# Performance work log

Hardware: AMD Instinct MI355X
Metric: run time of the kernel (lower is better)

Reference implementation:

```python
import jax, jax.numpy as jnp
import numpy as np
from jax import lax

T, B, DIN, H, OUT, L = 256, 128, 20, 1024, 1095, 3


def setup_inputs() -> dict:
    key = jax.random.key(0)
    ks = jax.random.split(key, 8)
    x = jax.random.normal(ks[0], (T, B, DIN), dtype=jnp.float32)
    c = jnp.zeros((L, B, H), dtype=jnp.float32)  # accepted but unused, as in original
    s_in = 1.0 / np.sqrt(DIN)
    s_h = 1.0 / np.sqrt(H)
    W1 = jax.random.uniform(ks[1], (DIN, H), jnp.float32, -s_in, s_in)
    b1 = jnp.zeros((H,), jnp.float32)
    # SRU per-layer weights: W maps h -> [z | f_pre | r_pre] (3H); biases for f and r gates
    W_sru = jax.random.uniform(ks[2], (L, H, 3 * H), jnp.float32, -s_h, s_h)
    bf_sru = jnp.zeros((L, H), jnp.float32)
    br_sru = jnp.zeros((L, H), jnp.float32)
    W3 = jax.random.uniform(ks[3], (H, OUT), jnp.float32, -s_h, s_h)
    b3 = jnp.zeros((OUT,), jnp.float32)
    return {"x": x, "c": c, "W1": W1, "b1": b1, "W_sru": W_sru,
            "bf_sru": bf_sru, "br_sru": br_sru, "W3": W3, "b3": b3}


def _sru_layer(h, W, bf, br):
    """One SRU layer. h: (T,B,H). Returns (h_out (T,B,H), c_final (B,H))."""
    U = jnp.einsum('tbh,hk->tbk', h, W)                    # (T,B,3H) big GEMM up front
    z, f_pre, r_pre = jnp.split(U, 3, axis=-1)
    f = jax.nn.sigmoid(f_pre + bf)
    r = jax.nn.sigmoid(r_pre + br)

    def step(c_prev, inp):
        f_t, z_t, r_t, x_t = inp
        c_t = f_t * c_prev + (1.0 - f_t) * z_t
        h_t = r_t * c_t + (1.0 - r_t) * x_t               # highway (input_size == hidden_size)
        return c_t, h_t

    c0 = jnp.zeros(h.shape[1:], h.dtype)
    c_final, h_out = lax.scan(step, c0, (f, z, r, h))
    return h_out, c_final


def reference(x, c, W1, b1, W_sru, bf_sru, br_sru, W3, b3):
    t, b, _ = x.shape
    h = (x.reshape(t * b, -1) @ W1 + b1).reshape(t, b, H)  # Dense_layer1
    c_finals = []
    for l in range(L):                                      # 3 SRU layers (fixed count)
        h, c_l = _sru_layer(h, W_sru[l], bf_sru[l], br_sru[l])
        c_finals.append(c_l)
    out = h.reshape(t * b, H) @ W3 + b3                     # Dense_layer3 -> (T*B, OUT)
    return out, jnp.stack(c_finals)                         # ((T*B,OUT), (L,B,H))
```

## Files before the change

kernel.cpp:

```cpp
#include <hip/hip_runtime.h>
#include <hip/hip_bf16.h>


#define T_DIM 256
#define B_DIM 128
#define DIN 20
#define H_DIM 1024
#define OUT_DIM 1095
#define L_DIM 3
#define M_DIM (T_DIM * B_DIM)
#define H3 (3 * H_DIM)
#define OUT_ELEMS ((size_t)M_DIM * OUT_DIM)

typedef __bf16 bf16x8 __attribute__((ext_vector_type(8)));
typedef __bf16 bf16x4 __attribute__((ext_vector_type(4)));
typedef __bf16 bf16x2 __attribute__((ext_vector_type(2)));
typedef float f32x4 __attribute__((ext_vector_type(4)));

__device__ __forceinline__ void async16(const __bf16* g, __bf16* l) {
  __builtin_amdgcn_global_load_lds(
      (const __attribute__((address_space(1))) void*)g,
      (__attribute__((address_space(3))) void*)l, 16, 0, 0);
}

__global__ void transpose_sru(const float* __restrict__ W, __bf16* __restrict__ Wt) {
  __shared__ float tile[32][33];
  int l = blockIdx.z;
  int j0 = blockIdx.x * 32;
  int i0 = blockIdx.y * 32;
  int tx = threadIdx.x, ty = threadIdx.y;
  const float* Wl = W + (size_t)l * H_DIM * H3;
  __bf16* Wtl = Wt + (size_t)l * H_DIM * H3;
#pragma unroll
  for (int r = 0; r < 4; r++)
    tile[ty + r * 8][tx] = Wl[(size_t)(i0 + ty + r * 8) * H3 + j0 + tx];
  __syncthreads();
#pragma unroll
  for (int r = 0; r < 4; r++)
    Wtl[(size_t)(j0 + ty + r * 8) * H_DIM + i0 + tx] = (__bf16)tile[tx][ty + r * 8];
}

__global__ void transpose_w3(const float* __restrict__ W, __bf16* __restrict__ Wt) {
  __shared__ float tile[32][33];
  int j0 = blockIdx.x * 32;
  int i0 = blockIdx.y * 32;
  int tx = threadIdx.x, ty = threadIdx.y;
#pragma unroll
  for (int r = 0; r < 4; r++) {
    int j = j0 + tx;
    if (j < OUT_DIM)
      tile[ty + r * 8][tx] = W[(size_t)(i0 + ty + r * 8) * OUT_DIM + j];
  }
  __syncthreads();
#pragma unroll
  for (int r = 0; r < 4; r++) {
    int j = j0 + ty + r * 8;
    if (j < OUT_DIM)
      Wt[(size_t)j * H_DIM + i0 + tx] = (__bf16)tile[tx][ty + r * 8];
  }
}

__global__ __launch_bounds__(256) void dense1(const float* __restrict__ x,
                                              const float* __restrict__ W1,
                                              const float* __restrict__ b1,
                                              __bf16* __restrict__ h) {
  __shared__ float wsl[DIN * 256];
  __shared__ float xs[128 * DIN];
  int tid = threadIdx.x;
  int m0 = blockIdx.x * 128;
  int n0 = blockIdx.y * 256;
#pragma unroll
  for (int k = 0; k < DIN; k++) wsl[k * 256 + tid] = W1[k * H_DIM + n0 + tid];
  for (int idx = tid; idx < 128 * DIN; idx += 256) xs[idx] = x[(size_t)m0 * DIN + idx];
  __syncthreads();
  float wreg[DIN];
#pragma unroll
  for (int k = 0; k < DIN; k++) wreg[k] = wsl[k * 256 + tid];
  float bias = b1[n0 + tid];
  for (int m = 0; m < 128; m++) {
    float acc = bias;
#pragma unroll
    for (int k = 0; k < DIN; k++) acc += xs[m * DIN + k] * wreg[k];
    h[(size_t)(m0 + m) * H_DIM + n0 + tid] = (__bf16)acc;
  }
}


template <int MH>
__device__ __forceinline__ void mfma16(f32x4 (&acc)[8][4], const bf16x8 (&aF)[4],
                                       const bf16x8 (&bF)[4]) {
  __builtin_amdgcn_s_setprio(1);
#pragma unroll
  for (int i = 0; i < 4; ++i)
#pragma unroll
    for (int fn = 0; fn < 4; ++fn)
      acc[MH * 4 + i][fn] =
          __builtin_amdgcn_mfma_f32_16x16x32_bf16(bF[fn], aF[i], acc[MH * 4 + i][fn], 0, 0, 0);
  __builtin_amdgcn_s_setprio(0);
}

__global__ __launch_bounds__(512, 2) void gemm_gate(const __bf16* __restrict__ A,
                                                    const __bf16* __restrict__ Bt,
                                                    __bf16* __restrict__ U,
                                                    const float* __restrict__ biasf,
                                                    const float* __restrict__ biasr) {
  __shared__ __align__(16) char lds[131072];
  int tid = threadIdx.x;
  int lane = tid & 63;
  int w = tid >> 6;
  int wm = w & 1, wn = w >> 1;

  int gx = gridDim.x;
  int lin = blockIdx.y * gx + blockIdx.x;
  int xcd = lin & 7;
  int kk = lin >> 3;
  int bx, by;
  if ((gx >> 3) == 8) { bx = xcd * 8 + (kk & 7); by = kk >> 3; }
  else                { bx = xcd * 4 + (kk & 3); by = kk >> 2; }
  int m0 = bx * 256, n0 = by * 256;

  int r8row = w * 8 + (lane >> 3);
  int cse = (lane & 7) * 8;
  int l15 = lane & 15;
  int quad = lane >> 4;

  f32x4 acc[8][4];
#pragma unroll
  for (int i = 0; i < 8; ++i)
#pragma unroll
    for (int j = 0; j < 4; ++j) acc[i][j] = (f32x4)0.f;
  bf16x8 aF[4], bF[4];

#define STAGE_TILE(T_) do { int _t = (T_); int _b = (_t & 1) * 65536;            \
    _Pragma("unroll") for (int _u = 0; _u < 4; ++_u)                             \
      async16(A + (size_t)(m0 + _u * 64 + r8row) * 1024 + _t * 64 + cse,         \
              (__bf16*)(lds + _b + _u * 8192 + w * 1024));                       \
    _Pragma("unroll") for (int _u = 0; _u < 4; ++_u)                             \
      async16(Bt + (size_t)(n0 + _u * 64 + r8row) * 1024 + _t * 64 + cse,        \
              (__bf16*)(lds + _b + 32768 + _u * 8192 + w * 1024)); } while (0)

#define LOAD_A(MH_, KS_) do {                                                    \
    _Pragma("unroll") for (int i = 0; i < 4; ++i)                                \
      aF[i] = *(const bf16x8*)(lds + bufc +                                      \
                (wm * 128 + (MH_) * 64 + i * 16 + l15) * 128 +                   \
                quad * 16 + (KS_) * 64); } while (0)

#define LOAD_B(KS_) do {                                                         \
    _Pragma("unroll") for (int i = 0; i < 4; ++i)                                \
      bF[i] = *(const bf16x8*)(lds + bufc + 32768 +                              \
                (wn * 64 + i * 16 + l15) * 128 +                                 \
                quad * 16 + (KS_) * 64); } while (0)

  STAGE_TILE(0);
  __syncthreads();

#pragma unroll 2
  for (int t = 0; t < 16; ++t) {
    int bufc = (t & 1) * 65536;
    if (t < 15) STAGE_TILE(t + 1);
    LOAD_B(0);
    LOAD_A(0, 0); mfma16<0>(acc, aF, bF);
    LOAD_A(1, 0); mfma16<1>(acc, aF, bF);
    LOAD_B(1);
    LOAD_A(0, 1); mfma16<0>(acc, aF, bF);
    LOAD_A(1, 1); mfma16<1>(acc, aF, bF);
    __syncthreads();
  }
#undef STAGE_TILE
#undef LOAD_A
#undef LOAD_B

  int gN[4];
  f32x4 bV[4];
#pragma unroll
  for (int fn = 0; fn < 4; ++fn) {
    int gc = n0 + wn * 64 + fn * 16 + quad * 4;
    int g = gc >> 10;
    gN[fn] = g;
    if (g == 1) bV[fn] = *(const f32x4*)&biasf[gc - 1024];
    else if (g == 2) bV[fn] = *(const f32x4*)&biasr[gc - 2048];
    else bV[fn] = (f32x4)0.f;
  }
#pragma unroll
  for (int fm = 0; fm < 8; ++fm) {
    int m = wm * 128 + fm * 16 + l15;
    char* rowp = lds + m * 512;
    int msw = (m & 7) << 4;
#pragma unroll
    for (int fn = 0; fn < 4; ++fn) {
      int nq = wn * 64 + fn * 16 + quad * 4;
      f32x4 v = acc[fm][fn];
      if (gN[fn] != 0) {
#pragma unroll
        for (int j = 0; j < 4; ++j) v[j] = 1.f / (1.f + __expf(-(v[j] + bV[fn][j])));
      }
      bf16x4 o;
#pragma unroll
      for (int j = 0; j < 4; ++j) o[j] = (__bf16)v[j];
      *(bf16x4*)(rowp + ((nq * 2) ^ msw)) = o;
    }
  }
  __syncthreads();
#pragma unroll
  for (int it = 0; it < 16; ++it) {
    int idx = it * 512 + tid;
    int row = idx >> 5;
    int ce = (idx & 31) * 8;
    bf16x8 val = *(const bf16x8*)(lds + row * 512 + ((ce * 2) ^ ((row & 7) << 4)));
    *(bf16x8*)&U[(size_t)(m0 + row) * H3 + n0 + ce] = val;
  }
}

__global__ __launch_bounds__(256) void gemm_out(const __bf16* __restrict__ A,
                                                const __bf16* __restrict__ Bt,
                                                float* __restrict__ C,
                                                const float* __restrict__ bias0) {
  constexpr int K = 1024;
  __shared__ __align__(16) __bf16 sA[128 * 32];
  __shared__ __align__(16) __bf16 sB[128 * 32];
  int tid = threadIdx.x;
  int lane = tid & 63;
  int wave = tid >> 6;
  int wm = wave & 1, wn = wave >> 1;
  int m0 = blockIdx.x * 128;
  int n0 = blockIdx.y * 128;

  f32x4 acc[4][4];
#pragma unroll
  for (int i = 0; i < 4; i++)
#pragma unroll
    for (int j = 0; j < 4; j++) acc[i][j] = (f32x4)0.f;

  int lrow = lane >> 2;
  int lcol8 = (lane & 3) * 8;
  int q8 = (lane >> 4) * 8;
  int l15 = lane & 15;

  for (int k0 = 0; k0 < K; k0 += 32) {
    __syncthreads();
#pragma unroll
    for (int i = 0; i < 2; i++) {
      int j = wave * 2 + i;
      int arow = m0 + j * 16 + lrow;
      async16(A + (size_t)arow * K + k0 + lcol8, &sA[j * 512]);
      int brow = n0 + j * 16 + lrow;
      brow = brow < OUT_DIM - 1 ? brow : OUT_DIM - 1;
      async16(Bt + (size_t)brow * K + k0 + lcol8, &sB[j * 512]);
    }
    __syncthreads();
    bf16x8 aF[4], bF[4];
#pragma unroll
    for (int i = 0; i < 4; i++) {
      aF[i] = *(const bf16x8*)&sA[(wm * 64 + i * 16 + l15) * 32 + q8];
      bF[i] = *(const bf16x8*)&sB[(wn * 64 + i * 16 + l15) * 32 + q8];
    }
#pragma unroll
    for (int mi = 0; mi < 4; mi++)
#pragma unroll
      for (int ni = 0; ni < 4; ni++)
        acc[mi][ni] = __builtin_amdgcn_mfma_f32_16x16x32_bf16(aF[mi], bF[ni], acc[mi][ni], 0, 0, 0);
  }

  int quad = lane >> 4;
#pragma unroll
  for (int mi = 0; mi < 4; mi++) {
    int rowBase = m0 + wm * 64 + mi * 16 + quad * 4;
#pragma unroll
    for (int ni = 0; ni < 4; ni++) {
      int col = n0 + wn * 64 + ni * 16 + l15;
      if (col < OUT_DIM) {
        float badd = bias0[col];
#pragma unroll
        for (int r = 0; r < 4; r++)
          C[(size_t)(rowBase + r) * OUT_DIM + col] = acc[mi][ni][r] + badd;
      }
    }
  }
}

__global__ __launch_bounds__(256) void sru_scan(const __bf16* __restrict__ U,
                                                __bf16* __restrict__ h,
                                                float* __restrict__ cst,
                                                float* __restrict__ cfin,
                                                int tc, int first, int last) {
  int id = blockIdx.x * 256 + threadIdx.x;
  int n2 = id * 2;
  int b = n2 >> 10;
  int hh = n2 & 1023;
  float c0, c1;
  if (first) { c0 = 0.f; c1 = 0.f; }
  else { c0 = cst[n2]; c1 = cst[n2 + 1]; }
  size_t ub = (size_t)b * H3 + hh;
  size_t xb = (size_t)b * H_DIM + hh;
  const size_t strideU = (size_t)B_DIM * H3;
  const size_t strideH = (size_t)B_DIM * H_DIM;
  for (int t = 0; t < tc; t++) {
    bf16x2 z2 = *(const bf16x2*)&U[ub];
    bf16x2 f2 = *(const bf16x2*)&U[ub + 1024];
    bf16x2 r2 = *(const bf16x2*)&U[ub + 2048];
    bf16x2 x2 = *(const bf16x2*)&h[xb];
    float f0 = (float)f2[0], f1 = (float)f2[1];
    float r0 = (float)r2[0], r1 = (float)r2[1];
    c0 = f0 * c0 + (1.f - f0) * (float)z2[0];
    c1 = f1 * c1 + (1.f - f1) * (float)z2[1];
    float h0 = r0 * c0 + (1.f - r0) * (float)x2[0];
    float h1 = r1 * c1 + (1.f - r1) * (float)x2[1];
    bf16x2 o;
    o[0] = (__bf16)h0;
    o[1] = (__bf16)h1;
    *(bf16x2*)&h[xb] = o;
    ub += strideU;
    xb += strideH;
  }
  cst[n2] = c0;
  cst[n2 + 1] = c1;
  if (last) {
    cfin[n2] = c0;
    cfin[n2 + 1] = c1;
  }
}

extern "C" void kernel_launch(void* const* d_in, const int* in_sizes, int n_in,
                              void* d_out, int out_size, void* d_ws, size_t ws_size,
                              hipStream_t stream) {
  const float* x = (const float*)d_in[0];
  const float* W1 = (const float*)d_in[2];
  const float* b1 = (const float*)d_in[3];
  const float* Wsru = (const float*)d_in[4];
  const float* bf_s = (const float*)d_in[5];
  const float* br_s = (const float*)d_in[6];
  const float* W3 = (const float*)d_in[7];
  const float* b3 = (const float*)d_in[8];
  float* out = (float*)d_out;

  const size_t kFixed = 67108864ull + 18874368ull + 2242560ull + 524288ull;
  int tch = (ws_size >= kFixed + (size_t)128 * B_DIM * H3 * 2) ? 128 : 64;
  int mch = tch * B_DIM;
  int nch = T_DIM / tch;

  char* wsb = (char*)d_ws;
  __bf16* h = (__bf16*)(wsb);
  __bf16* U = (__bf16*)(wsb + 67108864);
  char* wAfter = wsb + 67108864 + (size_t)mch * H3 * 2;
  __bf16* Wt = (__bf16*)(wAfter);
  __bf16* W3t = (__bf16*)(wAfter + 18874368);
  float* cst = (float*)(wAfter + 18874368 + 2242560);

  transpose_sru<<<dim3(H3 / 32, H_DIM / 32, L_DIM), dim3(32, 8), 0, stream>>>(Wsru, Wt);
  transpose_w3<<<dim3((OUT_DIM + 31) / 32, H_DIM / 32), dim3(32, 8), 0, stream>>>(W3, W3t);
  dense1<<<dim3(M_DIM / 128, H_DIM / 256), 256, 0, stream>>>(x, W1, b1, h);

  for (int l = 0; l < L_DIM; l++) {
    const __bf16* Wtl = Wt + (size_t)l * H_DIM * H3;
    const float* bfl = bf_s + l * H_DIM;
    const float* brl = br_s + l * H_DIM;
    float* cfin = out + OUT_ELEMS + (size_t)l * B_DIM * H_DIM;
    for (int ch = 0; ch < nch; ch++) {
      __bf16* hA = h + (size_t)ch * mch * H_DIM;
      gemm_gate<<<dim3(mch / 256, H3 / 256), 512, 0, stream>>>(hA, Wtl, U, bfl, brl);
      sru_scan<<<dim3(B_DIM * H_DIM / 512), 256, 0, stream>>>(
          U, hA, cst, cfin, tch, ch == 0 ? 1 : 0, ch == (nch - 1) ? 1 : 0);
    }
  }

  gemm_out<<<dim3(M_DIM / 128, (OUT_DIM + 127) / 128), 256, 0, stream>>>(h, W3t, out, b3);
}
```

Baseline: 1.341 ms.

## Deepen gate GEMM pipeline to four stages with swizzled LDS and vmcnt waits

The gate GEMM main loop moves from a double-buffered K=64 tile to a four-buffer K=32 ring with three tiles in flight. It uses explicit s_waitcnt vmcnt counts and bare s_barrier in place of __syncthreads. The LDS staging layout is XOR-swizzled so that fragment reads avoid bank conflicts. The aim is to hide global-load latency and cut LDS conflicts, at the cost of twice as many barriers per K and fragile hand-tuned wait counts.

```diff
diff --git a/kernel.cpp b/kernel.cpp
--- a/kernel.cpp
+++ b/kernel.cpp
@@ -23,6 +23,12 @@
       (__attribute__((address_space(3))) void*)l, 16, 0, 0);
 }
 
+__device__ __forceinline__ void bar() {
+  asm volatile("" ::: "memory");
+  __builtin_amdgcn_s_barrier();
+  asm volatile("" ::: "memory");
+}
+
 __global__ void transpose_sru(const float* __restrict__ W, __bf16* __restrict__ Wt) {
   __shared__ float tile[32][33];
   int l = blockIdx.z;
@@ -85,19 +91,6 @@
   }
 }
 
-
-template <int MH>
-__device__ __forceinline__ void mfma16(f32x4 (&acc)[8][4], const bf16x8 (&aF)[4],
-                                       const bf16x8 (&bF)[4]) {
-  __builtin_amdgcn_s_setprio(1);
-#pragma unroll
-  for (int i = 0; i < 4; ++i)
-#pragma unroll
-    for (int fn = 0; fn < 4; ++fn)
-      acc[MH * 4 + i][fn] =
-          __builtin_amdgcn_mfma_f32_16x16x32_bf16(bF[fn], aF[i], acc[MH * 4 + i][fn], 0, 0, 0);
-  __builtin_amdgcn_s_setprio(0);
-}
 
 __global__ __launch_bounds__(512, 2) void gemm_gate(const __bf16* __restrict__ A,
                                                     const __bf16* __restrict__ Bt,
@@ -119,56 +112,66 @@
   else                { bx = xcd * 4 + (kk & 3); by = kk >> 2; }
   int m0 = bx * 256, n0 = by * 256;
 
-  int r8row = w * 8 + (lane >> 3);
-  int cse = (lane & 7) * 8;
+  int su = tid >> 3;
+  int ssl = (tid & 7) ^ (su & 7);
+  int srow = 2 * su + (ssl >> 2);
+  int skel = (ssl & 3) * 8;
+
   int l15 = lane & 15;
   int quad = lane >> 4;
+  int rpl = l15 >> 1;
+  int innerA = ((((l15 & 1) << 6) | (quad << 4)) ^ (rpl << 4));
 
   f32x4 acc[8][4];
 #pragma unroll
   for (int i = 0; i < 8; ++i)
 #pragma unroll
     for (int j = 0; j < 4; ++j) acc[i][j] = (f32x4)0.f;
-  bf16x8 aF[4], bF[4];
-
-#define STAGE_TILE(T_) do { int _t = (T_); int _b = (_t & 1) * 65536;            \
-    _Pragma("unroll") for (int _u = 0; _u < 4; ++_u)                             \
-      async16(A + (size_t)(m0 + _u * 64 + r8row) * 1024 + _t * 64 + cse,         \
-              (__bf16*)(lds + _b + _u * 8192 + w * 1024));                       \
-    _Pragma("unroll") for (int _u = 0; _u < 4; ++_u)                             \
-      async16(Bt + (size_t)(n0 + _u * 64 + r8row) * 1024 + _t * 64 + cse,        \
-              (__bf16*)(lds + _b + 32768 + _u * 8192 + w * 1024)); } while (0)
-
-#define LOAD_A(MH_, KS_) do {                                                    \
-    _Pragma("unroll") for (int i = 0; i < 4; ++i)                                \
-      aF[i] = *(const bf16x8*)(lds + bufc +                                      \
-                (wm * 128 + (MH_) * 64 + i * 16 + l15) * 128 +                   \
-                quad * 16 + (KS_) * 64); } while (0)
-
-#define LOAD_B(KS_) do {                                                         \
-    _Pragma("unroll") for (int i = 0; i < 4; ++i)                                \
-      bF[i] = *(const bf16x8*)(lds + bufc + 32768 +                              \
-                (wn * 64 + i * 16 + l15) * 128 +                                 \
-                quad * 16 + (KS_) * 64); } while (0)
-
-  STAGE_TILE(0);
-  __syncthreads();
-
-#pragma unroll 2
-  for (int t = 0; t < 16; ++t) {
-    int bufc = (t & 1) * 65536;
-    if (t < 15) STAGE_TILE(t + 1);
-    LOAD_B(0);
-    LOAD_A(0, 0); mfma16<0>(acc, aF, bF);
-    LOAD_A(1, 0); mfma16<1>(acc, aF, bF);
-    LOAD_B(1);
-    LOAD_A(0, 1); mfma16<0>(acc, aF, bF);
-    LOAD_A(1, 1); mfma16<1>(acc, aF, bF);
-    __syncthreads();
-  }
-#undef STAGE_TILE
-#undef LOAD_A
-#undef LOAD_B
+
+#define STAGE(T_) do { int _t = (T_); int _bb = (_t & 3) * 32768;               \
+    _Pragma("unroll") for (int _p = 0; _p < 2; ++_p) {                          \
+      async16(A + (size_t)(m0 + _p * 128 + srow) * 1024 + _t * 32 + skel,       \
+              (__bf16*)(lds + _bb + _p * 8192 + tid * 16));                     \
+      async16(Bt + (size_t)(n0 + _p * 128 + srow) * 1024 + _t * 32 + skel,      \
+              (__bf16*)(lds + _bb + 16384 + _p * 8192 + tid * 16));             \
+    } } while (0)
+
+#define COMPUTE(BUFB) do {                                                      \
+    bf16x8 bF[4];                                                               \
+    _Pragma("unroll") for (int fn = 0; fn < 4; ++fn)                            \
+      bF[fn] = *(const bf16x8*)(lds + (BUFB) + 16384 +                          \
+                 (wn * 32 + fn * 8 + rpl) * 128 + innerA);                      \
+    __builtin_amdgcn_s_setprio(1);                                              \
+    _Pragma("unroll") for (int fm = 0; fm < 8; ++fm) {                          \
+      bf16x8 aF = *(const bf16x8*)(lds + (BUFB) +                               \
+                 (wm * 64 + fm * 8 + rpl) * 128 + innerA);                      \
+      _Pragma("unroll") for (int fn = 0; fn < 4; ++fn)                          \
+        acc[fm][fn] = __builtin_amdgcn_mfma_f32_16x16x32_bf16(bF[fn], aF,       \
+                          acc[fm][fn], 0, 0, 0);                                \
+    }                                                                           \
+    __builtin_amdgcn_s_setprio(0);                                              \
+  } while (0)
+
+  STAGE(0); STAGE(1); STAGE(2);
+  asm volatile("s_waitcnt vmcnt(8)" ::: "memory");
+  bar();
+
+  for (int t = 0; t < 29; ++t) {
+    STAGE(t + 3);
+    COMPUTE((t & 3) * 32768);
+    asm volatile("s_waitcnt vmcnt(8)" ::: "memory");
+    bar();
+  }
+  COMPUTE((29 & 3) * 32768);
+  asm volatile("s_waitcnt vmcnt(4)" ::: "memory");
+  bar();
+  COMPUTE((30 & 3) * 32768);
+  asm volatile("s_waitcnt vmcnt(0)" ::: "memory");
+  bar();
+  COMPUTE((31 & 3) * 32768);
+  bar();
+#undef STAGE
+#undef COMPUTE
 
   int gN[4];
   f32x4 bV[4];
@@ -200,7 +203,7 @@
       *(bf16x4*)(rowp + ((nq * 2) ^ msw)) = o;
     }
   }
-  __syncthreads();
+  bar();
 #pragma unroll
   for (int it = 0; it < 16; ++it) {
     int idx = it * 512 + tid;
```

Result: no change. 1.331 ms (-0.7%).
